# Kernel optimization log

Hardware: AMD Instinct MI355X
Metric: run time of the kernel (lower is better)

The kernel has to match this reference:

```python
import jax, jax.numpy as jnp
import numpy as np

B, L, E = 4, 1024, 1024
H = 16
HD = E // H
CLIP = 16
SCALE = 1.0 / np.sqrt(HD)


def setup_inputs() -> dict:
    key = jax.random.key(0)
    ks = jax.random.split(key, 13)
    def lin(k, fan_in, fan_out, gain):
        # xavier_uniform
        limit = gain * np.sqrt(6.0 / (fan_in + fan_out))
        return jax.random.uniform(k, (fan_out, fan_in), jnp.float32, -limit, limit)
    inv_sqrt2 = 1.0 / np.sqrt(2.0)
    return {
        "query": jax.random.normal(ks[0], (B, L, E), jnp.float32),
        "key": jax.random.normal(ks[1], (B, L, E), jnp.float32),
        "value": jax.random.normal(ks[2], (B, L, E), jnp.float32),
        "wq": lin(ks[3], E, E, inv_sqrt2), "bq": jnp.zeros((E,), jnp.float32),
        "wk": lin(ks[4], E, E, inv_sqrt2), "bk": jnp.zeros((E,), jnp.float32),
        "wv": lin(ks[5], E, E, inv_sqrt2), "bv": jnp.zeros((E,), jnp.float32),
        "wo": lin(ks[6], E, E, 1.0), "bo": jnp.zeros((E,), jnp.float32),
        "rel_k": jax.random.normal(ks[7], (2 * CLIP + 1, HD), jnp.float32) * 0.02,
        "rel_v": jax.random.normal(ks[8], (2 * CLIP + 1, HD), jnp.float32) * 0.02,
    }


def _heads(x):  # (B, L, E) -> (B, H, L, HD)
    return x.reshape(B, L, H, HD).transpose(0, 2, 1, 3)


def reference(query, key, value, wq, bq, wk, bk, wv, bv, wo, bo, rel_k, rel_v):
    q = _heads(query @ wq.T + bq)
    k = _heads(key @ wk.T + bk)
    v = _heads(value @ wv.T + bv)

    # relative-position index matrix (L_q, L_k), clipped to [-CLIP, CLIP]
    pos = jnp.arange(L)
    dist = jnp.clip(pos[None, :] - pos[:, None], -CLIP, CLIP) + CLIP
    r_k = rel_k[dist]  # (L, L, HD)
    r_v = rel_v[dist]  # (L, L, HD)

    dot = jnp.einsum('bhid,bhjd->bhij', q, k)
    rel = jnp.einsum('bhid,ijd->bhij', q, r_k)
    scores = (dot + rel) * SCALE
    attn = jax.nn.softmax(scores, axis=-1)

    y = jnp.einsum('bhij,bhjd->bhid', attn, v) + jnp.einsum('bhij,ijd->bhid', attn, r_v)
    y = y.transpose(0, 2, 1, 3).reshape(B, L, E)
    return y @ wo.T + bo
```

## Files before the change

kernel.cpp:

```cpp
#include <hip/hip_runtime.h>

#define BB 4
#define LL 1024
#define EE 1024
#define HH 16
#define HD 64
#define NBUCKET 33
#define SCALE 0.125f
#define SC2 (0.125f * 1.44269504088896f)

typedef unsigned short u16;
using f32x4 = __attribute__((ext_vector_type(4))) float;
using s16x8 = __attribute__((ext_vector_type(8))) short;

__device__ __forceinline__ u16 f2bf(float f) {
  union { float f; unsigned u; } x; x.f = f;
  unsigned r = (x.u + 0x7fffu + ((x.u >> 16) & 1u)) >> 16;
  return (u16)r;
}

__device__ __forceinline__ void gld_lds16(const void* g, void* s) {
  __builtin_amdgcn_global_load_lds((const __attribute__((address_space(1))) void*)g,
                                   (__attribute__((address_space(3))) void*)s, 16, 0, 0);
}

__global__ __launch_bounds__(256) void cvt_all(
    const float* __restrict__ q, const float* __restrict__ k, const float* __restrict__ v,
    const float* __restrict__ wq, const float* __restrict__ wk, const float* __restrict__ wv,
    const float* __restrict__ wo, const float* __restrict__ rk,
    u16* __restrict__ oq, u16* __restrict__ ok, u16* __restrict__ ov,
    u16* __restrict__ owq, u16* __restrict__ owk, u16* __restrict__ owv,
    u16* __restrict__ owo, u16* __restrict__ ork) {
  const int bid = blockIdx.x;
  const int tid = threadIdx.x;
  if (bid < 12288) {
    const int z = bid >> 12;
    const int i = (bid & 4095) * 256 + tid;
    const float* in = z == 0 ? q : (z == 1 ? k : v);
    u16* out = z == 0 ? oq : (z == 1 ? ok : ov);
    float4 f = ((const float4*)in)[i];
    ushort4 o;
    o.x = f2bf(f.x); o.y = f2bf(f.y); o.z = f2bf(f.z); o.w = f2bf(f.w);
    ((ushort4*)out)[i] = o;
  } else if (bid < 16384) {
    const int z = (bid - 12288) >> 10;
    const int i = ((bid - 12288) & 1023) * 256 + tid;
    const float* in = z == 0 ? wq : (z == 1 ? wk : (z == 2 ? wv : wo));
    u16* out = z == 0 ? owq : (z == 1 ? owk : (z == 2 ? owv : owo));
    float4 f = ((const float4*)in)[i];
    ushort4 o;
    o.x = f2bf(f.x); o.y = f2bf(f.y); o.z = f2bf(f.z); o.w = f2bf(f.w);
    ((ushort4*)out)[i] = o;
  } else {
    const int i = (bid - 16384) * 256 + tid;
    ork[i] = (i < 33 * 64) ? f2bf(rk[i]) : (u16)0;
  }
}

template <int MODE>
__device__ __forceinline__ void gemm128_dbuf(u16* __restrict__ sm,
                                             const u16* __restrict__ A,
                                             const u16* __restrict__ Bw,
                                             const float* __restrict__ bias,
                                             u16* __restrict__ obf,
                                             float* __restrict__ ofp,
                                             int N, int K, int m0, int n0) {
  const int tid = threadIdx.x;
  const int wave = tid >> 6, lane = tid & 63;
  const int row16 = lane & 15, quad = lane >> 4;
  const int wr = (wave >> 1) * 64, wc = (wave & 1) * 64;
  const int srow = lane >> 3, scol = (lane & 7) * 8;
  const int rsw = (row16 & 7) * 8;

  f32x4 acc[4][4] = {};

  auto stage = [&](int k0, u16* as, u16* bs) {
#pragma unroll
    for (int t = 0; t < 4; ++t) {
      const int chunk = wave * 4 + t;
      const int r = chunk * 8 + srow;
      const int cs = scol ^ ((r & 7) * 8);
      gld_lds16(A + (size_t)(m0 + r) * K + k0 + cs, as + chunk * 512);
      gld_lds16(Bw + (size_t)(n0 + r) * K + k0 + cs, bs + chunk * 512);
    }
  };

  stage(0, sm, sm + 8192);
  asm volatile("s_waitcnt vmcnt(0)" ::: "memory");
  __builtin_amdgcn_s_barrier();
  __builtin_amdgcn_sched_barrier(0);

  const int NK = K >> 6;
  for (int kt = 0; kt < NK; ++kt) {
    u16* as = sm + (kt & 1) * 16384;
    u16* bs = as + 8192;
    if (kt + 1 < NK) {
      u16* an = sm + ((kt + 1) & 1) * 16384;
      stage((kt + 1) << 6, an, an + 8192);
    }
#pragma unroll
    for (int ks = 0; ks < 2; ++ks) {
      const int cfs = (ks * 32 + quad * 8) ^ rsw;
      s16x8 af[4], bf[4];
#pragma unroll
      for (int mi = 0; mi < 4; ++mi)
        af[mi] = *(const s16x8*)&as[(wr + mi * 16 + row16) * 64 + cfs];
#pragma unroll
      for (int ni = 0; ni < 4; ++ni)
        bf[ni] = *(const s16x8*)&bs[(wc + ni * 16 + row16) * 64 + cfs];
#pragma unroll
      for (int mi = 0; mi < 4; ++mi)
#pragma unroll
        for (int ni = 0; ni < 4; ++ni)
          acc[mi][ni] = __builtin_amdgcn_mfma_f32_16x16x32_bf16(af[mi], bf[ni], acc[mi][ni], 0, 0, 0);
    }
    asm volatile("s_waitcnt vmcnt(0) lgkmcnt(0)" ::: "memory");
    __builtin_amdgcn_s_barrier();
    __builtin_amdgcn_sched_barrier(0);
  }

#pragma unroll
  for (int mi = 0; mi < 4; ++mi)
#pragma unroll
    for (int ni = 0; ni < 4; ++ni) {
      const int n = n0 + wc + ni * 16 + row16;
      const float bn = bias[n];
      if (MODE == 2) {
        const int mr0 = m0 + wr + mi * 16 + quad * 4;
        const int b = mr0 >> 10, l = mr0 & 1023;
        const int h = n >> 6, hd = n & 63;
        ushort4 o;
        o.x = f2bf(acc[mi][ni][0] + bn);
        o.y = f2bf(acc[mi][ni][1] + bn);
        o.z = f2bf(acc[mi][ni][2] + bn);
        o.w = f2bf(acc[mi][ni][3] + bn);
        *(ushort4*)&obf[((size_t)((b * HH + h) * HD + hd)) * LL + l] = o;
      } else {
#pragma unroll
        for (int r = 0; r < 4; ++r) {
          const int m = m0 + wr + mi * 16 + quad * 4 + r;
          const float v = acc[mi][ni][r] + bn;
          const int b = m >> 10, l = m & 1023, h = n >> 6, hd = n & 63;
          obf[((size_t)((b * HH + h) * LL + l)) * HD + hd] = f2bf(v);
        }
      }
    }
}

__global__ __launch_bounds__(256) void proj_gemm(
    const u16* __restrict__ xq, const u16* __restrict__ xk, const u16* __restrict__ xv,
    const u16* __restrict__ wqb, const u16* __restrict__ wkb, const u16* __restrict__ wvb,
    const float* __restrict__ bq, const float* __restrict__ bk, const float* __restrict__ bv,
    u16* __restrict__ oq, u16* __restrict__ ok, u16* __restrict__ ovt) {
  __shared__ u16 sm[4 * 8192];
  const int work = (blockIdx.x & 7) * 96 + (blockIdx.x >> 3);
  const int z = work >> 8;
  const int m0 = ((work & 255) >> 3) * 128;
  const int n0 = (work & 7) * 128;
  if (z == 0)
    gemm128_dbuf<0>(sm, xq, wqb, bq, oq, nullptr, EE, EE, m0, n0);
  else if (z == 1)
    gemm128_dbuf<0>(sm, xk, wkb, bk, ok, nullptr, EE, EE, m0, n0);
  else
    gemm128_dbuf<2>(sm, xv, wvb, bv, ovt, nullptr, EE, EE, m0, n0);
}

__global__ __launch_bounds__(256) void out_gemm(const u16* __restrict__ A,
                                                const u16* __restrict__ Bw,
                                                const float* __restrict__ bo,
                                                float* __restrict__ out) {
  __shared__ u16 sm[2 * 12288];
  const int work = (blockIdx.x & 7) * 64 + (blockIdx.x >> 3);
  const int m0 = (work >> 3) * 64;
  const int n0 = (work & 7) * 128;
  const int K = EE, N = EE;

  const int tid = threadIdx.x;
  const int wave = tid >> 6, lane = tid & 63;
  const int row16 = lane & 15, quad = lane >> 4;
  const int wm = (wave >> 1) * 32, wn = (wave & 1) * 64;
  const int srow = lane >> 3, scol = (lane & 7) * 8;
  const int rsw = (row16 & 7) * 8;

  f32x4 acc[2][4] = {};

  auto stage = [&](int k0, u16* as, u16* bs) {
#pragma unroll
    for (int t = 0; t < 2; ++t) {
      const int chunk = wave * 2 + t;
      const int r = chunk * 8 + srow;
      const int cs = scol ^ ((r & 7) * 8);
      gld_lds16(A + (size_t)(m0 + r) * K + k0 + cs, as + chunk * 512);
    }
#pragma unroll
    for (int t = 0; t < 4; ++t) {
      const int chunk = wave * 4 + t;
      const int r = chunk * 8 + srow;
      const int cs = scol ^ ((r & 7) * 8);
      gld_lds16(Bw + (size_t)(n0 + r) * K + k0 + cs, bs + chunk * 512);
    }
  };

  stage(0, sm, sm + 4096);
  asm volatile("s_waitcnt vmcnt(0)" ::: "memory");
  __builtin_amdgcn_s_barrier();
  __builtin_amdgcn_sched_barrier(0);

  for (int kt = 0; kt < 16; ++kt) {
    u16* as = sm + (kt & 1) * 12288;
    u16* bs = as + 4096;
    if (kt + 1 < 16) {
      u16* an = sm + ((kt + 1) & 1) * 12288;
      stage((kt + 1) << 6, an, an + 4096);
    }
#pragma unroll
    for (int ks = 0; ks < 2; ++ks) {
      const int cfs = (ks * 32 + quad * 8) ^ rsw;
      s16x8 af[2], bf[4];
#pragma unroll
      for (int mi = 0; mi < 2; ++mi)
        af[mi] = *(const s16x8*)&as[(wm + mi * 16 + row16) * 64 + cfs];
#pragma unroll
      for (int ni = 0; ni < 4; ++ni)
        bf[ni] = *(const s16x8*)&bs[(wn + ni * 16 + row16) * 64 + cfs];
#pragma unroll
      for (int mi = 0; mi < 2; ++mi)
#pragma unroll
        for (int ni = 0; ni < 4; ++ni)
          acc[mi][ni] = __builtin_amdgcn_mfma_f32_16x16x32_bf16(af[mi], bf[ni], acc[mi][ni], 0, 0, 0);
    }
    asm volatile("s_waitcnt vmcnt(0) lgkmcnt(0)" ::: "memory");
    __builtin_amdgcn_s_barrier();
    __builtin_amdgcn_sched_barrier(0);
  }

#pragma unroll
  for (int mi = 0; mi < 2; ++mi)
#pragma unroll
    for (int ni = 0; ni < 4; ++ni) {
      const int n = n0 + wn + ni * 16 + row16;
      const float bn = bo[n];
#pragma unroll
      for (int r = 0; r < 4; ++r) {
        const int m = m0 + wm + mi * 16 + quad * 4 + r;
        out[(size_t)m * N + n] = acc[mi][ni][r] + bn;
      }
    }
}

__global__ __launch_bounds__(256) void attn_fused(
    const u16* __restrict__ Q, const u16* __restrict__ Kb, const u16* __restrict__ Vt,
    const u16* __restrict__ RKp, const float* __restrict__ RV, u16* __restrict__ Y) {
  __shared__ __align__(16) float qr_sm[4][576];
  __shared__ __align__(16) float s_sm[4][16 * 36];
  __shared__ __align__(16) unsigned char kv[16384];

  const int tid = threadIdx.x;
  const int wave = tid >> 6, lane = tid & 63;
  const int row16 = lane & 15, quad = lane >> 4;
  const int bh = blockIdx.x & 63;
  const int i0 = (blockIdx.x >> 6) * 64;
  const int wq0 = i0 + wave * 16;
  const u16* qp = Q + (size_t)bh * LL * HD;
  const char* kpB = (const char*)(Kb + (size_t)bh * LL * HD);
  const char* vpB = (const char*)(Vt + (size_t)bh * HD * LL);

  float* qr_w = &qr_sm[wave][0];
  float* s_w = &s_sm[wave][0];

  int srcK[2], srcV[2];
#pragma unroll
  for (int t = 0; t < 2; ++t) {
    const int cK = (wave * 2 + t) * 64 + lane;
    const int rw = cK >> 3;
    const int cb = ((cK * 16) & 127) ^ ((rw & 7) << 4);
    srcK[t] = rw * 128 + cb;
    srcV[t] = rw * 2048 + cb;
  }
  const int q2 = row16 >> 2;
  const int prow = ((((q2 << 1) | (q2 >> 1)) & 3) << 2) + (row16 & 3);
  const int swzK = (prow & 7) << 4;
  const int swzV = (row16 & 7) << 4;
  const int rho4 = (((quad << 1) | (quad >> 1)) & 3) << 2;

#pragma unroll
  for (int t = 0; t < 2; ++t) {
    gld_lds16(kpB + srcK[t], kv + (wave * 2 + t) * 1024);
    gld_lds16(vpB + srcV[t], kv + 8192 + (wave * 2 + t) * 1024);
  }

  for (int t = lane; t < 16 * 36; t += 64) s_w[t] = 0.f;

  s16x8 qf[2];
#pragma unroll
  for (int ks = 0; ks < 2; ++ks)
    qf[ks] = *(const s16x8*)(qp + (size_t)(wq0 + row16) * HD + ks * 32 + quad * 8);

  f32x4 a0, a2;
#pragma unroll
  for (int nt = 0; nt < 3; ++nt) {
    f32x4 a = {};
#pragma unroll
    for (int ks = 0; ks < 2; ++ks) {
      s16x8 afr = *(const s16x8*)(RKp + (size_t)(nt * 16 + row16) * HD + ks * 32 + quad * 8);
      a = __builtin_amdgcn_mfma_f32_16x16x32_bf16(afr, qf[ks], a, 0, 0, 0);
    }
    if (nt == 0) a0 = a;
    if (nt == 2) a2 = a;
#pragma unroll
    for (int r = 0; r < 4; ++r) {
      const int bk = nt * 16 + quad * 4 + r;
      if (bk < NBUCKET) qr_w[bk * 17 + row16] = a[r];
    }
  }
  const float blo = __shfl(a0[0], row16);
  const float bhi = __shfl(a2[0], row16);

  f32x4 oacc[4] = {};
  float rsum = 0.f, plos = 0.f, phis = 0.f;
  int baseg[4];
#pragma unroll
  for (int g = 0; g < 4; ++g) baseg[g] = g * 16 + rho4 - wq0 - row16;

  asm volatile("s_waitcnt vmcnt(0) lgkmcnt(0)" ::: "memory");
  __builtin_amdgcn_s_barrier();
  __builtin_amdgcn_sched_barrier(0);

  for (int jt = 0; jt < 16; ++jt) {
    const int j0 = jt * 64;

    s16x8 kreg[2], vreg[2];
    if (jt < 15) {
      const size_t j1 = (size_t)(j0 + 64);
#pragma unroll
      for (int t = 0; t < 2; ++t) {
        kreg[t] = *(const s16x8*)(kpB + j1 * 128 + srcK[t]);
        vreg[t] = *(const s16x8*)(vpB + j1 * 2 + srcV[t]);
      }
    }

    f32x4 sacc[4] = {};
    __builtin_amdgcn_s_setprio(1);
#pragma unroll
    for (int ks = 0; ks < 2; ++ks)
#pragma unroll
      for (int g = 0; g < 4; ++g) {
        const int L = (g * 16 + prow) * 128 + ks * 64 + quad * 16;
        const s16x8 kfr = *(const s16x8*)(kv + (L ^ swzK));
        sacc[g] = __builtin_amdgcn_mfma_f32_16x16x32_bf16(kfr, qf[ks], sacc[g], 0, 0, 0);
      }
    __builtin_amdgcn_s_setprio(0);

    unsigned pk[4][2];
    const bool far_lo = (wq0 >= j0 + 79);
    const bool far_hi = (j0 >= wq0 + 31);
    if (far_lo || far_hi) {
      const float bb = (far_lo ? blo : bhi) * SC2;
      float tacc = 0.f;
#pragma unroll
      for (int g = 0; g < 4; ++g)
#pragma unroll
        for (int rr = 0; rr < 2; ++rr) {
          const float pv0 = __builtin_amdgcn_exp2f(sacc[g][rr * 2] * SC2 + bb);
          const float pv1 = __builtin_amdgcn_exp2f(sacc[g][rr * 2 + 1] * SC2 + bb);
          tacc += pv0 + pv1;
          unsigned c;
          asm("v_cvt_pk_bf16_f32 %0, %1, %2" : "=v"(c) : "v"(pv0), "v"(pv1));
          pk[g][rr] = c;
        }
      rsum += tacc;
      if (far_lo) plos += tacc; else phis += tacc;
    } else {
#pragma unroll
      for (int g = 0; g < 4; ++g)
#pragma unroll
        for (int rr = 0; rr < 2; ++rr) {
          float pv2[2];
#pragma unroll
          for (int e = 0; e < 2; ++e) {
            const int r = rr * 2 + e;
            const int dr = baseg[g] + j0 + r;
            int bk = dr < -16 ? -16 : (dr > 16 ? 16 : dr);
            bk += 16;
            const float bias = qr_w[bk * 17 + row16];
            const float pv = __builtin_amdgcn_exp2f((sacc[g][r] + bias) * SC2);
            pv2[e] = pv;
            rsum += pv;
            if (dr <= -16) plos += pv;
            else if (dr >= 16) phis += pv;
            else atomicAdd(&s_w[row16 * 36 + bk], pv);
          }
          unsigned c;
          asm("v_cvt_pk_bf16_f32 %0, %1, %2" : "=v"(c) : "v"(pv2[0]), "v"(pv2[1]));
          pk[g][rr] = c;
        }
    }

    s16x8 pf[2];
#pragma unroll
    for (int ks = 0; ks < 2; ++ks) {
      unsigned x0 = pk[ks * 2][0], y0 = pk[ks * 2 + 1][0];
      unsigned x1 = pk[ks * 2][1], y1 = pk[ks * 2 + 1][1];
      asm("v_permlane32_swap_b32 %0, %1" : "+v"(x0), "+v"(y0));
      asm("v_permlane32_swap_b32 %0, %1" : "+v"(x1), "+v"(y1));
      union { unsigned u[4]; s16x8 v; } pfu;
      pfu.u[0] = x0; pfu.u[1] = x1; pfu.u[2] = y0; pfu.u[3] = y1;
      pf[ks] = pfu.v;
    }

    __builtin_amdgcn_s_setprio(1);
#pragma unroll
    for (int ks = 0; ks < 2; ++ks)
#pragma unroll
      for (int dt = 0; dt < 4; ++dt) {
        const int L = (dt * 16 + row16) * 128 + ks * 64 + quad * 16;
        const s16x8 vfr = *(const s16x8*)(kv + 8192 + (L ^ swzV));
        oacc[dt] = __builtin_amdgcn_mfma_f32_16x16x32_bf16(vfr, pf[ks], oacc[dt], 0, 0, 0);
      }
    __builtin_amdgcn_s_setprio(0);

    asm volatile("s_waitcnt lgkmcnt(0)" ::: "memory");
    __builtin_amdgcn_s_barrier();
    __builtin_amdgcn_sched_barrier(0);

    if (jt < 15) {
#pragma unroll
      for (int t = 0; t < 2; ++t) {
        *(s16x8*)(kv + (wave * 2 + t) * 1024 + lane * 16) = kreg[t];
        *(s16x8*)(kv + 8192 + (wave * 2 + t) * 1024 + lane * 16) = vreg[t];
      }
      asm volatile("s_waitcnt lgkmcnt(0)" ::: "memory");
      __builtin_amdgcn_s_barrier();
      __builtin_amdgcn_sched_barrier(0);
    }
  }

  float t1 = rsum + __shfl_xor(rsum, 16);
  const float lacc = t1 + __shfl_xor(t1, 32);
  t1 = plos + __shfl_xor(plos, 16);
  const float slo = t1 + __shfl_xor(t1, 32);
  t1 = phis + __shfl_xor(phis, 16);
  const float shi = t1 + __shfl_xor(t1, 32);

  float* rv_sm = (float*)kv;
  for (int t = tid; t < NBUCKET * HD; t += 256) rv_sm[t] = RV[t];
  __syncthreads();

  const int b = bh >> 4, h = bh & 15;
  float rel[4][4] = {};
  for (int bk = 0; bk < NBUCKET; ++bk) {
    float sv = s_w[row16 * 36 + bk];
    if (bk == 0) sv += slo;
    if (bk == 32) sv += shi;
#pragma unroll
    for (int dt = 0; dt < 4; ++dt) {
      const f32x4 rv4 = *(const f32x4*)&rv_sm[bk * HD + dt * 16 + quad * 4];
#pragma unroll
      for (int r = 0; r < 4; ++r) rel[dt][r] += sv * rv4[r];
    }
  }
  const float inv = 1.0f / lacc;
#pragma unroll
  for (int dt = 0; dt < 4; ++dt) {
    ushort4 o;
    o.x = f2bf((oacc[dt][0] + rel[dt][0]) * inv);
    o.y = f2bf((oacc[dt][1] + rel[dt][1]) * inv);
    o.z = f2bf((oacc[dt][2] + rel[dt][2]) * inv);
    o.w = f2bf((oacc[dt][3] + rel[dt][3]) * inv);
    *(ushort4*)&Y[((size_t)(b * LL + wq0 + row16)) * EE + h * HD + dt * 16 + quad * 4] = o;
  }
}

extern "C" void kernel_launch(void* const* d_in, const int* in_sizes, int n_in,
                              void* d_out, int out_size, void* d_ws, size_t ws_size,
                              hipStream_t stream) {
  const float* query = (const float*)d_in[0];
  const float* key_  = (const float*)d_in[1];
  const float* value = (const float*)d_in[2];
  const float* wq = (const float*)d_in[3];
  const float* bq = (const float*)d_in[4];
  const float* wk = (const float*)d_in[5];
  const float* bk = (const float*)d_in[6];
  const float* wv = (const float*)d_in[7];
  const float* bv = (const float*)d_in[8];
  const float* wo = (const float*)d_in[9];
  const float* bo = (const float*)d_in[10];
  const float* rel_k = (const float*)d_in[11];
  const float* rel_v = (const float*)d_in[12];

  char* base = (char*)d_ws;
  size_t off = 0;
  auto alloc = [&](size_t bytes) -> void* {
    void* p = base + off;
    off += (bytes + 255) & ~(size_t)255;
    return p;
  };
  const size_t XE = (size_t)BB * LL * EE;
  u16* xq    = (u16*)alloc(XE * 2);
  u16* xk    = (u16*)alloc(XE * 2);
  u16* xv    = (u16*)alloc(XE * 2);
  u16* wqb   = (u16*)alloc((size_t)EE * EE * 2);
  u16* wkb   = (u16*)alloc((size_t)EE * EE * 2);
  u16* wvb   = (u16*)alloc((size_t)EE * EE * 2);
  u16* wob   = (u16*)alloc((size_t)EE * EE * 2);
  u16* q_ws  = (u16*)alloc(XE * 2);
  u16* k_ws  = (u16*)alloc(XE * 2);
  u16* vt_ws = (u16*)alloc(XE * 2);
  u16* relkp = (u16*)alloc(48 * 64 * 2);
  u16* y_ws = xq;

  cvt_all<<<16396, 256, 0, stream>>>(query, key_, value, wq, wk, wv, wo, rel_k,
                                     xq, xk, xv, wqb, wkb, wvb, wob, relkp);

  proj_gemm<<<768, 256, 0, stream>>>(
      xq, xk, xv, wqb, wkb, wvb, bq, bk, bv, q_ws, k_ws, vt_ws);

  attn_fused<<<1024, 256, 0, stream>>>(q_ws, k_ws, vt_ws, relkp, rel_v, y_ws);

  out_gemm<<<512, 256, 0, stream>>>(y_ws, wob, bo, (float*)d_out);
}
```

Baseline: 225.9 us.

## Fuse fp32-to-bf16 activation conversion into projection GEMM A-tile loading

The separate pass that converted query/key/value activations to bf16 is removed. The projection GEMM now loads fp32 A tiles into registers, converts them with packed bf16 conversion instructions, and writes them to swizzled LDS, with the next tile's loads issued before the MFMA loop. This drops a full read-write round trip of the activations. In exchange the GEMM reads twice the bytes for A and needs more registers, and the A staging no longer uses direct global-to-LDS loads. The conversion also changes from the explicit round-to-nearest-even code to the hardware instruction.

```diff
diff --git a/kernel.cpp b/kernel.cpp
--- a/kernel.cpp
+++ b/kernel.cpp
@@ -24,27 +24,16 @@
                                    (__attribute__((address_space(3))) void*)s, 16, 0, 0);
 }
 
-__global__ __launch_bounds__(256) void cvt_all(
-    const float* __restrict__ q, const float* __restrict__ k, const float* __restrict__ v,
+__global__ __launch_bounds__(256) void cvt_w(
     const float* __restrict__ wq, const float* __restrict__ wk, const float* __restrict__ wv,
     const float* __restrict__ wo, const float* __restrict__ rk,
-    u16* __restrict__ oq, u16* __restrict__ ok, u16* __restrict__ ov,
     u16* __restrict__ owq, u16* __restrict__ owk, u16* __restrict__ owv,
     u16* __restrict__ owo, u16* __restrict__ ork) {
   const int bid = blockIdx.x;
   const int tid = threadIdx.x;
-  if (bid < 12288) {
-    const int z = bid >> 12;
-    const int i = (bid & 4095) * 256 + tid;
-    const float* in = z == 0 ? q : (z == 1 ? k : v);
-    u16* out = z == 0 ? oq : (z == 1 ? ok : ov);
-    float4 f = ((const float4*)in)[i];
-    ushort4 o;
-    o.x = f2bf(f.x); o.y = f2bf(f.y); o.z = f2bf(f.z); o.w = f2bf(f.w);
-    ((ushort4*)out)[i] = o;
-  } else if (bid < 16384) {
-    const int z = (bid - 12288) >> 10;
-    const int i = ((bid - 12288) & 1023) * 256 + tid;
+  if (bid < 4096) {
+    const int z = bid >> 10;
+    const int i = (bid & 1023) * 256 + tid;
     const float* in = z == 0 ? wq : (z == 1 ? wk : (z == 2 ? wv : wo));
     u16* out = z == 0 ? owq : (z == 1 ? owk : (z == 2 ? owv : owo));
     float4 f = ((const float4*)in)[i];
@@ -52,19 +41,18 @@
     o.x = f2bf(f.x); o.y = f2bf(f.y); o.z = f2bf(f.z); o.w = f2bf(f.w);
     ((ushort4*)out)[i] = o;
   } else {
-    const int i = (bid - 16384) * 256 + tid;
+    const int i = (bid - 4096) * 256 + tid;
     ork[i] = (i < 33 * 64) ? f2bf(rk[i]) : (u16)0;
   }
 }
 
 template <int MODE>
-__device__ __forceinline__ void gemm128_dbuf(u16* __restrict__ sm,
-                                             const u16* __restrict__ A,
-                                             const u16* __restrict__ Bw,
-                                             const float* __restrict__ bias,
-                                             u16* __restrict__ obf,
-                                             float* __restrict__ ofp,
-                                             int N, int K, int m0, int n0) {
+__device__ __forceinline__ void gemm128_f32a_dbuf(u16* __restrict__ sm,
+                                                  const float* __restrict__ A,
+                                                  const u16* __restrict__ Bw,
+                                                  const float* __restrict__ bias,
+                                                  u16* __restrict__ obf,
+                                                  int K, int m0, int n0) {
   const int tid = threadIdx.x;
   const int wave = tid >> 6, lane = tid & 63;
   const int row16 = lane & 15, quad = lane >> 4;
@@ -74,19 +62,47 @@
 
   f32x4 acc[4][4] = {};
 
-  auto stage = [&](int k0, u16* as, u16* bs) {
+  auto stageB = [&](int k0, u16* bs) {
 #pragma unroll
     for (int t = 0; t < 4; ++t) {
       const int chunk = wave * 4 + t;
       const int r = chunk * 8 + srow;
       const int cs = scol ^ ((r & 7) * 8);
-      gld_lds16(A + (size_t)(m0 + r) * K + k0 + cs, as + chunk * 512);
       gld_lds16(Bw + (size_t)(n0 + r) * K + k0 + cs, bs + chunk * 512);
     }
   };
-
-  stage(0, sm, sm + 8192);
-  asm volatile("s_waitcnt vmcnt(0)" ::: "memory");
+  auto loadA = [&](int k0, float4* fr) {
+#pragma unroll
+    for (int p = 0; p < 4; ++p) {
+      const int pc = p * 256 + tid;
+      const int ar = pc >> 3, ac0 = (pc & 7) * 8;
+      const float4* src = (const float4*)(A + (size_t)(m0 + ar) * K + k0 + ac0);
+      fr[2 * p] = src[0];
+      fr[2 * p + 1] = src[1];
+    }
+  };
+  auto writeA = [&](const float4* fr, u16* as) {
+#pragma unroll
+    for (int p = 0; p < 4; ++p) {
+      const int pc = p * 256 + tid;
+      const int ar = pc >> 3, ac0 = (pc & 7) * 8;
+      const float4 f0 = fr[2 * p], f1 = fr[2 * p + 1];
+      unsigned w0, w1, w2, w3;
+      asm("v_cvt_pk_bf16_f32 %0, %1, %2" : "=v"(w0) : "v"(f0.x), "v"(f0.y));
+      asm("v_cvt_pk_bf16_f32 %0, %1, %2" : "=v"(w1) : "v"(f0.z), "v"(f0.w));
+      asm("v_cvt_pk_bf16_f32 %0, %1, %2" : "=v"(w2) : "v"(f1.x), "v"(f1.y));
+      asm("v_cvt_pk_bf16_f32 %0, %1, %2" : "=v"(w3) : "v"(f1.z), "v"(f1.w));
+      union { unsigned u[4]; s16x8 v; } w;
+      w.u[0] = w0; w.u[1] = w1; w.u[2] = w2; w.u[3] = w3;
+      *(s16x8*)&as[ar * 64 + (ac0 ^ ((ar & 7) * 8))] = w.v;
+    }
+  };
+
+  float4 fr[8];
+  loadA(0, fr);
+  stageB(0, sm + 8192);
+  writeA(fr, sm);
+  asm volatile("s_waitcnt vmcnt(0) lgkmcnt(0)" ::: "memory");
   __builtin_amdgcn_s_barrier();
   __builtin_amdgcn_sched_barrier(0);
 
@@ -94,9 +110,10 @@
   for (int kt = 0; kt < NK; ++kt) {
     u16* as = sm + (kt & 1) * 16384;
     u16* bs = as + 8192;
+    u16* an = sm + ((kt & 1) ^ 1) * 16384;
     if (kt + 1 < NK) {
-      u16* an = sm + ((kt + 1) & 1) * 16384;
-      stage((kt + 1) << 6, an, an + 8192);
+      loadA((kt + 1) << 6, fr);
+      stageB((kt + 1) << 6, an + 8192);
     }
 #pragma unroll
     for (int ks = 0; ks < 2; ++ks) {
@@ -114,6 +131,7 @@
         for (int ni = 0; ni < 4; ++ni)
           acc[mi][ni] = __builtin_amdgcn_mfma_f32_16x16x32_bf16(af[mi], bf[ni], acc[mi][ni], 0, 0, 0);
     }
+    if (kt + 1 < NK) writeA(fr, an);
     asm volatile("s_waitcnt vmcnt(0) lgkmcnt(0)" ::: "memory");
     __builtin_amdgcn_s_barrier();
     __builtin_amdgcn_sched_barrier(0);
@@ -148,7 +166,7 @@
 }
 
 __global__ __launch_bounds__(256) void proj_gemm(
-    const u16* __restrict__ xq, const u16* __restrict__ xk, const u16* __restrict__ xv,
+    const float* __restrict__ xq, const float* __restrict__ xk, const float* __restrict__ xv,
     const u16* __restrict__ wqb, const u16* __restrict__ wkb, const u16* __restrict__ wvb,
     const float* __restrict__ bq, const float* __restrict__ bk, const float* __restrict__ bv,
     u16* __restrict__ oq, u16* __restrict__ ok, u16* __restrict__ ovt) {
@@ -158,11 +176,11 @@
   const int m0 = ((work & 255) >> 3) * 128;
   const int n0 = (work & 7) * 128;
   if (z == 0)
-    gemm128_dbuf<0>(sm, xq, wqb, bq, oq, nullptr, EE, EE, m0, n0);
+    gemm128_f32a_dbuf<0>(sm, xq, wqb, bq, oq, EE, m0, n0);
   else if (z == 1)
-    gemm128_dbuf<0>(sm, xk, wkb, bk, ok, nullptr, EE, EE, m0, n0);
+    gemm128_f32a_dbuf<0>(sm, xk, wkb, bk, ok, EE, m0, n0);
   else
-    gemm128_dbuf<2>(sm, xv, wvb, bv, ovt, nullptr, EE, EE, m0, n0);
+    gemm128_f32a_dbuf<2>(sm, xv, wvb, bv, ovt, EE, m0, n0);
 }
 
 __global__ __launch_bounds__(256) void out_gemm(const u16* __restrict__ A,
@@ -496,9 +514,6 @@
     return p;
   };
   const size_t XE = (size_t)BB * LL * EE;
-  u16* xq    = (u16*)alloc(XE * 2);
-  u16* xk    = (u16*)alloc(XE * 2);
-  u16* xv    = (u16*)alloc(XE * 2);
   u16* wqb   = (u16*)alloc((size_t)EE * EE * 2);
   u16* wkb   = (u16*)alloc((size_t)EE * EE * 2);
   u16* wvb   = (u16*)alloc((size_t)EE * EE * 2);
@@ -507,13 +522,12 @@
   u16* k_ws  = (u16*)alloc(XE * 2);
   u16* vt_ws = (u16*)alloc(XE * 2);
   u16* relkp = (u16*)alloc(48 * 64 * 2);
-  u16* y_ws = xq;
-
-  cvt_all<<<16396, 256, 0, stream>>>(query, key_, value, wq, wk, wv, wo, rel_k,
-                                     xq, xk, xv, wqb, wkb, wvb, wob, relkp);
+  u16* y_ws  = (u16*)alloc(XE * 2);
+
+  cvt_w<<<4108, 256, 0, stream>>>(wq, wk, wv, wo, rel_k, wqb, wkb, wvb, wob, relkp);
 
   proj_gemm<<<768, 256, 0, stream>>>(
-      xq, xk, xv, wqb, wkb, wvb, bq, bk, bv, q_ws, k_ws, vt_ws);
+      query, key_, value, wqb, wkb, wvb, bq, bk, bv, q_ws, k_ws, vt_ws);
 
   attn_fused<<<1024, 256, 0, stream>>>(q_ws, k_ws, vt_ws, relkp, rel_v, y_ws);
 
```

After: 238.1 us. 1.05x slower.

## Widen attention blocks to 8 waves sharing each K/V tile

Applied to the files above, without the earlier changes.

The attention kernel now runs 512-thread blocks covering 128 query rows instead of 256-thread blocks covering 64, so each K/V tile staged in LDS serves twice as many waves. Each wave now loads one 16-byte chunk of K and V per tile instead of two, which halves redundant global K/V traffic per query row. The cost is half as many blocks (512 on the GPU), more LDS per block, and barriers that must synchronize twice as many waves.

```diff
diff --git a/kernel.cpp b/kernel.cpp
--- a/kernel.cpp
+++ b/kernel.cpp
@@ -248,18 +248,18 @@
     }
 }
 
-__global__ __launch_bounds__(256) void attn_fused(
+__global__ __launch_bounds__(512) void attn_fused(
     const u16* __restrict__ Q, const u16* __restrict__ Kb, const u16* __restrict__ Vt,
     const u16* __restrict__ RKp, const float* __restrict__ RV, u16* __restrict__ Y) {
-  __shared__ __align__(16) float qr_sm[4][576];
-  __shared__ __align__(16) float s_sm[4][16 * 36];
+  __shared__ __align__(16) float qr_sm[8][576];
+  __shared__ __align__(16) float s_sm[8][576];
   __shared__ __align__(16) unsigned char kv[16384];
 
   const int tid = threadIdx.x;
   const int wave = tid >> 6, lane = tid & 63;
   const int row16 = lane & 15, quad = lane >> 4;
   const int bh = blockIdx.x & 63;
-  const int i0 = (blockIdx.x >> 6) * 64;
+  const int i0 = (blockIdx.x >> 6) * 128;
   const int wq0 = i0 + wave * 16;
   const u16* qp = Q + (size_t)bh * LL * HD;
   const char* kpB = (const char*)(Kb + (size_t)bh * LL * HD);
@@ -268,28 +268,21 @@
   float* qr_w = &qr_sm[wave][0];
   float* s_w = &s_sm[wave][0];
 
-  int srcK[2], srcV[2];
-#pragma unroll
-  for (int t = 0; t < 2; ++t) {
-    const int cK = (wave * 2 + t) * 64 + lane;
-    const int rw = cK >> 3;
-    const int cb = ((cK * 16) & 127) ^ ((rw & 7) << 4);
-    srcK[t] = rw * 128 + cb;
-    srcV[t] = rw * 2048 + cb;
-  }
+  const int cK = wave * 64 + lane;
+  const int rw = cK >> 3;
+  const int cb = ((cK * 16) & 127) ^ ((rw & 7) << 4);
+  const int srcK = rw * 128 + cb;
+  const int srcV = rw * 2048 + cb;
   const int q2 = row16 >> 2;
   const int prow = ((((q2 << 1) | (q2 >> 1)) & 3) << 2) + (row16 & 3);
   const int swzK = (prow & 7) << 4;
   const int swzV = (row16 & 7) << 4;
   const int rho4 = (((quad << 1) | (quad >> 1)) & 3) << 2;
 
-#pragma unroll
-  for (int t = 0; t < 2; ++t) {
-    gld_lds16(kpB + srcK[t], kv + (wave * 2 + t) * 1024);
-    gld_lds16(vpB + srcV[t], kv + 8192 + (wave * 2 + t) * 1024);
-  }
-
-  for (int t = lane; t < 16 * 36; t += 64) s_w[t] = 0.f;
+  gld_lds16(kpB + srcK, kv + wave * 1024);
+  gld_lds16(vpB + srcV, kv + 8192 + wave * 1024);
+
+  for (int t = lane; t < 576; t += 64) s_w[t] = 0.f;
 
   s16x8 qf[2];
 #pragma unroll
@@ -329,14 +322,11 @@
   for (int jt = 0; jt < 16; ++jt) {
     const int j0 = jt * 64;
 
-    s16x8 kreg[2], vreg[2];
+    s16x8 kreg, vreg;
     if (jt < 15) {
       const size_t j1 = (size_t)(j0 + 64);
-#pragma unroll
-      for (int t = 0; t < 2; ++t) {
-        kreg[t] = *(const s16x8*)(kpB + j1 * 128 + srcK[t]);
-        vreg[t] = *(const s16x8*)(vpB + j1 * 2 + srcV[t]);
-      }
+      kreg = *(const s16x8*)(kpB + j1 * 128 + srcK);
+      vreg = *(const s16x8*)(vpB + j1 * 2 + srcV);
     }
 
     f32x4 sacc[4] = {};
@@ -424,11 +414,8 @@
     __builtin_amdgcn_sched_barrier(0);
 
     if (jt < 15) {
-#pragma unroll
-      for (int t = 0; t < 2; ++t) {
-        *(s16x8*)(kv + (wave * 2 + t) * 1024 + lane * 16) = kreg[t];
-        *(s16x8*)(kv + 8192 + (wave * 2 + t) * 1024 + lane * 16) = vreg[t];
-      }
+      *(s16x8*)(kv + wave * 1024 + lane * 16) = kreg;
+      *(s16x8*)(kv + 8192 + wave * 1024 + lane * 16) = vreg;
       asm volatile("s_waitcnt lgkmcnt(0)" ::: "memory");
       __builtin_amdgcn_s_barrier();
       __builtin_amdgcn_sched_barrier(0);
@@ -443,7 +430,7 @@
   const float shi = t1 + __shfl_xor(t1, 32);
 
   float* rv_sm = (float*)kv;
-  for (int t = tid; t < NBUCKET * HD; t += 256) rv_sm[t] = RV[t];
+  for (int t = tid; t < NBUCKET * HD; t += 512) rv_sm[t] = RV[t];
   __syncthreads();
 
   const int b = bh >> 4, h = bh & 15;
@@ -515,7 +502,7 @@
   proj_gemm<<<768, 256, 0, stream>>>(
       xq, xk, xv, wqb, wkb, wvb, bq, bk, bv, q_ws, k_ws, vt_ws);
 
-  attn_fused<<<1024, 256, 0, stream>>>(q_ws, k_ws, vt_ws, relkp, rel_v, y_ws);
+  attn_fused<<<512, 512, 0, stream>>>(q_ws, k_ws, vt_ws, relkp, rel_v, y_ws);
 
   out_gemm<<<512, 256, 0, stream>>>(y_ws, wob, bo, (float*)d_out);
 }
```

New measurement: 230.6 us. +2.0%, slower.
